# Performance work log

Measured on AMD Instinct MI355X. Metric: run time of the kernel, lower is better.

Reference implementation:

```python
import jax, jax.numpy as jnp
import numpy as np

GRID_SPACING = 1.0


def setup_inputs() -> dict:
    key = jax.random.key(0)
    k1, k2 = jax.random.split(key)
    B, H, W, D = 4, 128, 128, 128
    phi_positive = jax.random.normal(k1, (B, H, W, D), dtype=jnp.float32)
    phi_negative = jax.random.uniform(k2, (B, H, W, D), dtype=jnp.float32)
    lambda_repulsion = jnp.ones((1,), dtype=jnp.float32) * 2.0
    return {
        "phi_positive": phi_positive,
        "phi_negative": phi_negative,
        "lambda_repulsion": lambda_repulsion,
    }


def reference(phi_positive, phi_negative, lambda_repulsion):
    h = GRID_SPACING
    # Conformal factor Phi = phi+ - lambda * phi-
    Phi = phi_positive - lambda_repulsion[0] * phi_negative  # (B,H,W,D)
    # Single replicate-pad of Phi, reused for gradient and Laplacian stencils
    p = jnp.pad(Phi, ((0, 0), (1, 1), (1, 1), (1, 1)), mode="edge")
    xp = p[:, 2:, 1:-1, 1:-1]
    xm = p[:, :-2, 1:-1, 1:-1]
    yp = p[:, 1:-1, 2:, 1:-1]
    ym = p[:, 1:-1, :-2, 1:-1]
    zp = p[:, 1:-1, 1:-1, 2:]
    zm = p[:, 1:-1, 1:-1, :-2]
    inv2h = 1.0 / (2.0 * h)
    gx = (xp - xm) * inv2h
    gy = (yp - ym) * inv2h
    gz = (zp - zm) * inv2h
    grad_sq = gx * gx + gy * gy + gz * gz  # |grad Phi|^2
    lap = (xp + xm + yp + ym + zp + zm - 6.0 * Phi) / (h * h)
    # R = -2 e^{-2Phi} (lap Phi + 2 |grad Phi|^2)
    R = -2.0 * jnp.exp(-2.0 * Phi) * (lap + 2.0 * grad_sq)
    return R
```

## Files before the change

### kernel.cpp

```cpp
#include <hip/hip_runtime.h>


#define NVEC (4 * 128 * 128 * 32)

typedef float vfloat4 __attribute__((ext_vector_type(4)));

__global__ __launch_bounds__(256) void conformal_kernel(
    const float* __restrict__ pos, const float* __restrict__ neg,
    const float* __restrict__ lamp, float* __restrict__ out)
{
    const float lam = lamp[0];
    const int vid = blockIdx.x * blockDim.x + threadIdx.x;

    const int dvec = vid & 31;
    const int w    = (vid >> 5)  & 127;
    const int h    = (vid >> 12) & 127;

    const vfloat4* posv = (const vfloat4*)pos;
    const vfloat4* negv = (const vfloat4*)neg;

    const int i_yp = (w < 127) ? vid + 32   : vid;
    const int i_ym = (w > 0)   ? vid - 32   : vid;
    const int i_xp = (h < 127) ? vid + 4096 : vid;
    const int i_xm = (h > 0)   ? vid - 4096 : vid;

    vfloat4 p_c  = posv[vid],  n_c  = negv[vid];
    vfloat4 p_yp = posv[i_yp], n_yp = negv[i_yp];
    vfloat4 p_ym = posv[i_ym], n_ym = negv[i_ym];
    vfloat4 p_xp = posv[i_xp], n_xp = negv[i_xp];
    vfloat4 p_xm = posv[i_xm], n_xm = negv[i_xm];

    const vfloat4 cphi = p_c - lam * n_c;
    const float c0 = cphi.x, c1 = cphi.y, c2 = cphi.z, c3 = cphi.w;

    const float from_up   = __shfl_up(c3, 1);
    const float from_down = __shfl_down(c0, 1);
    const float left  = (dvec > 0)  ? from_up   : c0;
    const float right = (dvec < 31) ? from_down : c3;

    const vfloat4 xp = p_xp - lam * n_xp;
    const vfloat4 xm = p_xm - lam * n_xm;
    const vfloat4 yp = p_yp - lam * n_yp;
    const vfloat4 ym = p_ym - lam * n_ym;

    const float cc[4]  = { c0, c1, c2, c3 };
    const float zl[4]  = { left, c0, c1, c2 };
    const float zr[4]  = { c1, c2, c3, right };
    const float xpv[4] = { xp.x, xp.y, xp.z, xp.w };
    const float xmv[4] = { xm.x, xm.y, xm.z, xm.w };
    const float ypv[4] = { yp.x, yp.y, yp.z, yp.w };
    const float ymv[4] = { ym.x, ym.y, ym.z, ym.w };

    vfloat4 o;
#pragma unroll
    for (int j = 0; j < 4; ++j) {
        const float gx = (xpv[j] - xmv[j]) * 0.5f;
        const float gy = (ypv[j] - ymv[j]) * 0.5f;
        const float gz = (zr[j]  - zl[j])  * 0.5f;
        const float grad_sq = gx * gx + gy * gy + gz * gz;
        const float lap = xpv[j] + xmv[j] + ypv[j] + ymv[j] + zl[j] + zr[j]
                          - 6.0f * cc[j];
        o[j] = -2.0f * __expf(-2.0f * cc[j]) * (lap + 2.0f * grad_sq);
    }

    ((vfloat4*)out)[vid] = o;
}

extern "C" void kernel_launch(void* const* d_in, const int* in_sizes, int n_in,
                              void* d_out, int out_size, void* d_ws, size_t ws_size,
                              hipStream_t stream) {
    const float* pos = (const float*)d_in[0];
    const float* neg = (const float*)d_in[1];
    const float* lam = (const float*)d_in[2];
    float* out = (float*)d_out;

    const int threads = 256;
    const int blocks  = NVEC / threads;
    conformal_kernel<<<blocks, threads, 0, stream>>>(pos, neg, lam, out);
}
```

Before: 104.1 us.

## Compute 2x2 (h,w) output block per thread to reuse neighbor loads

```diff
diff --git a/kernel.cpp b/kernel.cpp
--- a/kernel.cpp
+++ b/kernel.cpp
@@ -1,69 +1,109 @@
 #include <hip/hip_runtime.h>
 
 
-#define NVEC (4 * 128 * 128 * 32)
-
 typedef float vfloat4 __attribute__((ext_vector_type(4)));
 
-__global__ __launch_bounds__(256) void conformal_kernel(
+#define NTHREADS (4 * 64 * 64 * 32)
+
+__device__ __forceinline__ vfloat4 stencil_out(
+    const vfloat4 c, const vfloat4 xpv, const vfloat4 xmv,
+    const vfloat4 ypv, const vfloat4 ymv, const int dvec)
+{
+    const float fu = __shfl_up(c.w, 1);
+    const float fd = __shfl_down(c.x, 1);
+    const float left  = (dvec > 0)  ? fu : c.x;
+    const float right = (dvec < 31) ? fd : c.w;
+
+    const float cc[4]  = { c.x, c.y, c.z, c.w };
+    const float zl[4]  = { left, c.x, c.y, c.z };
+    const float zr[4]  = { c.y, c.z, c.w, right };
+    const float xpa[4] = { xpv.x, xpv.y, xpv.z, xpv.w };
+    const float xma[4] = { xmv.x, xmv.y, xmv.z, xmv.w };
+    const float ypa[4] = { ypv.x, ypv.y, ypv.z, ypv.w };
+    const float yma[4] = { ymv.x, ymv.y, ymv.z, ymv.w };
+
+    vfloat4 o;
+#pragma unroll
+    for (int j = 0; j < 4; ++j) {
+        const float gx = (xpa[j] - xma[j]) * 0.5f;
+        const float gy = (ypa[j] - yma[j]) * 0.5f;
+        const float gz = (zr[j]  - zl[j])  * 0.5f;
+        const float grad_sq = gx * gx + gy * gy + gz * gz;
+        const float lap = xpa[j] + xma[j] + ypa[j] + yma[j] + zl[j] + zr[j]
+                          - 6.0f * cc[j];
+        o[j] = -2.0f * __expf(-2.0f * cc[j]) * (lap + 2.0f * grad_sq);
+    }
+    return o;
+}
+
+__global__ __launch_bounds__(256, 4) void conformal_kernel(
     const float* __restrict__ pos, const float* __restrict__ neg,
     const float* __restrict__ lamp, float* __restrict__ out)
 {
     const float lam = lamp[0];
-    const int vid = blockIdx.x * blockDim.x + threadIdx.x;
+    const int t = blockIdx.x * blockDim.x + threadIdx.x;
 
-    const int dvec = vid & 31;
-    const int w    = (vid >> 5)  & 127;
-    const int h    = (vid >> 12) & 127;
+    const int dvec = t & 31;
+    const int wp   = (t >> 5)  & 63;
+    const int hp   = (t >> 11) & 63;
+    const int b    = t >> 17;
+
+    const int w0 = wp * 2, w1 = w0 + 1;
+    const int h0 = hp * 2, h1 = h0 + 1;
+
+    const int hxm = (h0 > 0)   ? h0 - 1 : 0;
+    const int hxp = (h1 < 127) ? h1 + 1 : 127;
+    const int wym = (w0 > 0)   ? w0 - 1 : 0;
+    const int wyp = (w1 < 127) ? w1 + 1 : 127;
+
+    const int base = ((b * 128 + h0) * 128 + w0) * 32 + dvec;
+    const int i_c00 = base;
+    const int i_c01 = base + 32;
+    const int i_c10 = base + 4096;
+    const int i_c11 = base + 4096 + 32;
+    const int i_xm0 = ((b * 128 + hxm) * 128 + w0) * 32 + dvec;
+    const int i_xm1 = i_xm0 + 32;
+    const int i_xp0 = ((b * 128 + hxp) * 128 + w0) * 32 + dvec;
+    const int i_xp1 = i_xp0 + 32;
+    const int i_ym0 = ((b * 128 + h0) * 128 + wym) * 32 + dvec;
+    const int i_ym1 = i_ym0 + 4096;
+    const int i_yp0 = ((b * 128 + h0) * 128 + wyp) * 32 + dvec;
+    const int i_yp1 = i_yp0 + 4096;
 
     const vfloat4* posv = (const vfloat4*)pos;
     const vfloat4* negv = (const vfloat4*)neg;
 
-    const int i_yp = (w < 127) ? vid + 32   : vid;
-    const int i_ym = (w > 0)   ? vid - 32   : vid;
-    const int i_xp = (h < 127) ? vid + 4096 : vid;
-    const int i_xm = (h > 0)   ? vid - 4096 : vid;
+    const vfloat4 p_c00 = posv[i_c00], n_c00 = negv[i_c00];
+    const vfloat4 p_c01 = posv[i_c01], n_c01 = negv[i_c01];
+    const vfloat4 p_c10 = posv[i_c10], n_c10 = negv[i_c10];
+    const vfloat4 p_c11 = posv[i_c11], n_c11 = negv[i_c11];
+    const vfloat4 p_xm0 = posv[i_xm0], n_xm0 = negv[i_xm0];
+    const vfloat4 p_xm1 = posv[i_xm1], n_xm1 = negv[i_xm1];
+    const vfloat4 p_xp0 = posv[i_xp0], n_xp0 = negv[i_xp0];
+    const vfloat4 p_xp1 = posv[i_xp1], n_xp1 = negv[i_xp1];
+    const vfloat4 p_ym0 = posv[i_ym0], n_ym0 = negv[i_ym0];
+    const vfloat4 p_ym1 = posv[i_ym1], n_ym1 = negv[i_ym1];
+    const vfloat4 p_yp0 = posv[i_yp0], n_yp0 = negv[i_yp0];
+    const vfloat4 p_yp1 = posv[i_yp1], n_yp1 = negv[i_yp1];
 
-    vfloat4 p_c  = posv[vid],  n_c  = negv[vid];
-    vfloat4 p_yp = posv[i_yp], n_yp = negv[i_yp];
-    vfloat4 p_ym = posv[i_ym], n_ym = negv[i_ym];
-    vfloat4 p_xp = posv[i_xp], n_xp = negv[i_xp];
-    vfloat4 p_xm = posv[i_xm], n_xm = negv[i_xm];
+    const vfloat4 c00 = p_c00 - lam * n_c00;
+    const vfloat4 c01 = p_c01 - lam * n_c01;
+    const vfloat4 c10 = p_c10 - lam * n_c10;
+    const vfloat4 c11 = p_c11 - lam * n_c11;
+    const vfloat4 xm0 = p_xm0 - lam * n_xm0;
+    const vfloat4 xm1 = p_xm1 - lam * n_xm1;
+    const vfloat4 xp0 = p_xp0 - lam * n_xp0;
+    const vfloat4 xp1 = p_xp1 - lam * n_xp1;
+    const vfloat4 ym0 = p_ym0 - lam * n_ym0;
+    const vfloat4 ym1 = p_ym1 - lam * n_ym1;
+    const vfloat4 yp0 = p_yp0 - lam * n_yp0;
+    const vfloat4 yp1 = p_yp1 - lam * n_yp1;
 
-    const vfloat4 cphi = p_c - lam * n_c;
-    const float c0 = cphi.x, c1 = cphi.y, c2 = cphi.z, c3 = cphi.w;
-
-    const float from_up   = __shfl_up(c3, 1);
-    const float from_down = __shfl_down(c0, 1);
-    const float left  = (dvec > 0)  ? from_up   : c0;
-    const float right = (dvec < 31) ? from_down : c3;
-
-    const vfloat4 xp = p_xp - lam * n_xp;
-    const vfloat4 xm = p_xm - lam * n_xm;
-    const vfloat4 yp = p_yp - lam * n_yp;
-    const vfloat4 ym = p_ym - lam * n_ym;
-
-    const float cc[4]  = { c0, c1, c2, c3 };
-    const float zl[4]  = { left, c0, c1, c2 };
-    const float zr[4]  = { c1, c2, c3, right };
-    const float xpv[4] = { xp.x, xp.y, xp.z, xp.w };
-    const float xmv[4] = { xm.x, xm.y, xm.z, xm.w };
-    const float ypv[4] = { yp.x, yp.y, yp.z, yp.w };
-    const float ymv[4] = { ym.x, ym.y, ym.z, ym.w };
-
-    vfloat4 o;
-#pragma unroll
-    for (int j = 0; j < 4; ++j) {
-        const float gx = (xpv[j] - xmv[j]) * 0.5f;
-        const float gy = (ypv[j] - ymv[j]) * 0.5f;
-        const float gz = (zr[j]  - zl[j])  * 0.5f;
-        const float grad_sq = gx * gx + gy * gy + gz * gz;
-        const float lap = xpv[j] + xmv[j] + ypv[j] + ymv[j] + zl[j] + zr[j]
-                          - 6.0f * cc[j];
-        o[j] = -2.0f * __expf(-2.0f * cc[j]) * (lap + 2.0f * grad_sq);
-    }
-
-    ((vfloat4*)out)[vid] = o;
+    vfloat4* outv = (vfloat4*)out;
+    outv[i_c00] = stencil_out(c00,  c10,  xm0,  c01,  ym0, dvec);
+    outv[i_c01] = stencil_out(c01,  c11,  xm1,  yp0,  c00, dvec);
+    outv[i_c10] = stencil_out(c10,  xp0,  c00,  c11,  ym1, dvec);
+    outv[i_c11] = stencil_out(c11,  xp1,  c01,  yp1,  c10, dvec);
 }
 
 extern "C" void kernel_launch(void* const* d_in, const int* in_sizes, int n_in,
@@ -75,6 +115,6 @@
     float* out = (float*)d_out;
 
     const int threads = 256;
-    const int blocks  = NVEC / threads;
+    const int blocks  = NTHREADS / threads;
     conformal_kernel<<<blocks, threads, 0, stream>>>(pos, neg, lam, out);
 }
```

Result: no change. 102.8 us (-1.2%).
